# Performance work log

Hardware: AMD Instinct MI355X
Metric: run time of the kernel (lower is better)

## Reference

```python
import jax, jax.numpy as jnp
import numpy as np

B, D = 500000, 128
UNITS, STACK, NPRED = 4, 12, 2
EPS = 1e-3  # Keras BatchNormalization default epsilon


def setup_inputs() -> dict:
    key = jax.random.key(0)
    ks = jax.random.split(key, 2 * STACK + 4)
    inp = {"x": jax.random.normal(ks[0], (B, D), dtype=jnp.float32)}
    # 12 dense weights with growing input width D + 4*i
    for i in range(STACK):
        inp[f"w{i}"] = jax.random.normal(ks[1 + i], (D + UNITS * i, UNITS), dtype=jnp.float32) * 0.1
    inp["gamma"] = 1.0 + 0.1 * jax.random.normal(ks[STACK + 1], (STACK, UNITS), dtype=jnp.float32)
    inp["beta"] = 0.1 * jax.random.normal(ks[STACK + 2], (STACK, UNITS), dtype=jnp.float32)
    inp["mean"] = 0.1 * jax.random.normal(ks[STACK + 3], (STACK, UNITS), dtype=jnp.float32)
    inp["var"] = 0.5 + jax.random.uniform(ks[2 * STACK], (STACK, UNITS), dtype=jnp.float32)
    inp["wf"] = jax.random.normal(ks[2 * STACK + 1], (D + UNITS * STACK, NPRED), dtype=jnp.float32) * 0.1
    inp["bf"] = jnp.zeros((NPRED,), dtype=jnp.float32)
    return inp


def reference(x, w0, w1, w2, w3, w4, w5, w6, w7, w8, w9, w10, w11,
              gamma, beta, mean, var, wf, bf):
    ws = [w0, w1, w2, w3, w4, w5, w6, w7, w8, w9, w10, w11]
    h = x
    for i in range(STACK):
        y = h @ ws[i]  # [B, 4]
        # inference-mode BatchNorm, fused scale/shift
        scale = gamma[i] * jax.lax.rsqrt(var[i] + EPS)
        y = jax.nn.relu(y * scale + (beta[i] - mean[i] * scale))
        h = jnp.concatenate([y, h], axis=-1)  # width grows by 4
    logits = h @ wf + bf  # [B, 2]
    return jax.nn.softmax(logits, axis=-1)
```

## Files before the change

### kernel.cpp

```cpp
#include <hip/hip_runtime.h>

#define NROWS 500000
#define DD 128
#define NSTACK 12
#define BNEPS 1e-3f
#define NCOL 50
#define NTILES ((NROWS + 63) / 64)

typedef float  v2f    __attribute__((ext_vector_type(2)));
typedef float  v4f    __attribute__((ext_vector_type(4)));
typedef float  f32x4  __attribute__((ext_vector_type(4)));
typedef __bf16 bf16x8 __attribute__((ext_vector_type(8)));

__device__ __forceinline__ unsigned short f2bf_rn(float f) {
    unsigned u = __float_as_uint(f);
    return (unsigned short)((u + 0x7FFFu + ((u >> 16) & 1u)) >> 16);
}

__global__ __launch_bounds__(256, 3) void gemm_kernel(
    const float* __restrict__ x,
    const float* __restrict__ w0,  const float* __restrict__ w1,
    const float* __restrict__ w2,  const float* __restrict__ w3,
    const float* __restrict__ w4,  const float* __restrict__ w5,
    const float* __restrict__ w6,  const float* __restrict__ w7,
    const float* __restrict__ w8,  const float* __restrict__ w9,
    const float* __restrict__ w10, const float* __restrict__ w11,
    const float* __restrict__ wf,
    float* __restrict__ T)
{
    __shared__ __align__(16) unsigned short bsw[4][4][64][8];

    const int tid = threadIdx.x;
    const float* ws[NSTACK] = {w0,w1,w2,w3,w4,w5,w6,w7,w8,w9,w10,w11};

    for (int idx = tid; idx < 1024; idx += 256)
        ((f32x4*)&bsw[0][0][0][0])[idx] = (f32x4){0.f, 0.f, 0.f, 0.f};
    __syncthreads();

#pragma unroll
    for (int i = 0; i < NSTACK; ++i) {
        const float* wsi = ws[i];
        for (int e = tid; e < 512; e += 256) {
            const int k = e >> 2, u = e & 3;
            const int n = 4 * i + u;
            const int kt = k >> 5, q = (k >> 3) & 3, j = k & 7;
            const int nt = n >> 4, lane = q * 16 + (n & 15);
            bsw[kt][nt][lane][j] = f2bf_rn(wsi[16 * i + e]);
        }
    }
    {
        const int e = tid;
        const int k = e >> 1, u = e & 1;
        const int n = 48 + u;
        const int kt = k >> 5, q = (k >> 3) & 3, j = k & 7;
        const int lane = q * 16 + (n & 15);
        bsw[kt][3][lane][j] = f2bf_rn(wf[96 + e]);
    }
    __syncthreads();

    const int lane = tid & 63;
    const int wv   = tid >> 6;
    const int tile = blockIdx.x * 4 + wv;
    const int rowbase = tile * 64;
    const int m = lane & 15;
    const int q = lane >> 4;

    const float* arow[4];
#pragma unroll
    for (int mt = 0; mt < 4; ++mt) {
        int r = rowbase + mt * 16 + m;
        if (r > NROWS - 1) r = NROWS - 1;
        arow[mt] = x + (size_t)r * DD + q * 8;
    }

    f32x4 acc[4][4];
#pragma unroll
    for (int mt = 0; mt < 4; ++mt)
#pragma unroll
        for (int nt = 0; nt < 4; ++nt) acc[mt][nt] = (f32x4){0.f, 0.f, 0.f, 0.f};

    v4f A0[2][4], A1[2][4];
#pragma unroll
    for (int mt = 0; mt < 4; ++mt) {
        A0[0][mt] = *(const v4f*)(arow[mt]);
        A1[0][mt] = *(const v4f*)(arow[mt] + 4);
    }

#pragma unroll
    for (int kt = 0; kt < 4; ++kt) {
        const int cur = kt & 1, nxt = cur ^ 1;
        if (kt < 3) {
#pragma unroll
            for (int mt = 0; mt < 4; ++mt) {
                A0[nxt][mt] = *(const v4f*)(arow[mt] + (kt + 1) * 32);
                A1[nxt][mt] = *(const v4f*)(arow[mt] + (kt + 1) * 32 + 4);
            }
        }
        bf16x8 bfrag[4];
#pragma unroll
        for (int nt = 0; nt < 4; ++nt)
            bfrag[nt] = *(const bf16x8*)&bsw[kt][nt][lane][0];
#pragma unroll
        for (int mt = 0; mt < 4; ++mt) {
            union { unsigned short us[8]; bf16x8 bv; } au;
#pragma unroll
            for (int e = 0; e < 4; ++e) {
                au.us[e]     = f2bf_rn(A0[cur][mt][e]);
                au.us[4 + e] = f2bf_rn(A1[cur][mt][e]);
            }
#pragma unroll
            for (int nt = 0; nt < 4; ++nt)
                acc[mt][nt] = __builtin_amdgcn_mfma_f32_16x16x32_bf16(
                    au.bv, bfrag[nt], acc[mt][nt], 0, 0, 0);
        }
    }

    float* tb = T + (size_t)tile * 4096;
#pragma unroll
    for (int nt = 0; nt < 4; ++nt) {
        const int c = nt * 16 + m;
        if (c < NCOL) {
#pragma unroll
            for (int mt = 0; mt < 4; ++mt)
                *(v4f*)(tb + c * 64 + mt * 16 + q * 4) = acc[mt][nt];
        }
    }
}

__global__ __launch_bounds__(256, 4) void recur_kernel(
    const float* __restrict__ T,
    const float* __restrict__ w0,  const float* __restrict__ w1,
    const float* __restrict__ w2,  const float* __restrict__ w3,
    const float* __restrict__ w4,  const float* __restrict__ w5,
    const float* __restrict__ w6,  const float* __restrict__ w7,
    const float* __restrict__ w8,  const float* __restrict__ w9,
    const float* __restrict__ w10, const float* __restrict__ w11,
    const float* __restrict__ gamma_, const float* __restrict__ beta_,
    const float* __restrict__ mean_,  const float* __restrict__ var_,
    const float* __restrict__ wf,     const float* __restrict__ bf,
    float* __restrict__ out)
{
    const int row = blockIdx.x * blockDim.x + threadIdx.x;
    if (row >= NROWS) return;

    const float* ws[NSTACK] = {w0,w1,w2,w3,w4,w5,w6,w7,w8,w9,w10,w11};

    const int tile = row >> 6, rr = row & 63;
    const float* tb = T + (size_t)tile * 4096 + rr;

    float Tv[NCOL];
#pragma unroll
    for (int c = 0; c < NCOL; ++c) Tv[c] = tb[c * 64];

    float y[NSTACK * 4];
#pragma unroll
    for (int i = 0; i < NSTACK; ++i) {
        float a0 = Tv[4 * i + 0], a1 = Tv[4 * i + 1];
        float a2 = Tv[4 * i + 2], a3 = Tv[4 * i + 3];
        const float* wsi = ws[i];
#pragma unroll
        for (int mr = 0; mr < 4 * i; ++mr) {
            const float hv = y[(i - 1 - (mr >> 2)) * 4 + (mr & 3)];
            a0 += hv * wsi[4 * mr + 0];
            a1 += hv * wsi[4 * mr + 1];
            a2 += hv * wsi[4 * mr + 2];
            a3 += hv * wsi[4 * mr + 3];
        }
#pragma unroll
        for (int u = 0; u < 4; ++u) {
            const float sc = gamma_[4 * i + u] * __frsqrt_rn(var_[4 * i + u] + BNEPS);
            const float sh = beta_[4 * i + u] - mean_[4 * i + u] * sc;
            const float a  = (u == 0 ? a0 : u == 1 ? a1 : u == 2 ? a2 : a3);
            const float v  = a * sc + sh;
            y[4 * i + u] = v > 0.f ? v : 0.f;
        }
    }

    float l0 = Tv[48] + bf[0];
    float l1 = Tv[49] + bf[1];
#pragma unroll
    for (int mr = 0; mr < 48; ++mr) {
        const float hv = y[(11 - (mr >> 2)) * 4 + (mr & 3)];
        l0 += hv * wf[2 * mr + 0];
        l1 += hv * wf[2 * mr + 1];
    }

    const float mx = fmaxf(l0, l1);
    const float e0 = __expf(l0 - mx);
    const float e1 = __expf(l1 - mx);
    const float inv = 1.0f / (e0 + e1);
    *(v2f*)(out + (size_t)row * 2) = (v2f){e0 * inv, e1 * inv};
}

extern "C" void kernel_launch(void* const* d_in, const int* in_sizes, int n_in,
                              void* d_out, int out_size, void* d_ws, size_t ws_size,
                              hipStream_t stream) {
    const float* x   = (const float*)d_in[0];
    const float* w0  = (const float*)d_in[1];
    const float* w1  = (const float*)d_in[2];
    const float* w2  = (const float*)d_in[3];
    const float* w3  = (const float*)d_in[4];
    const float* w4  = (const float*)d_in[5];
    const float* w5  = (const float*)d_in[6];
    const float* w6  = (const float*)d_in[7];
    const float* w7  = (const float*)d_in[8];
    const float* w8  = (const float*)d_in[9];
    const float* w9  = (const float*)d_in[10];
    const float* w10 = (const float*)d_in[11];
    const float* w11 = (const float*)d_in[12];
    const float* gm  = (const float*)d_in[13];
    const float* bt  = (const float*)d_in[14];
    const float* mn  = (const float*)d_in[15];
    const float* vr  = (const float*)d_in[16];
    const float* wf  = (const float*)d_in[17];
    const float* bf  = (const float*)d_in[18];
    float* out = (float*)d_out;
    float* T   = (float*)d_ws;

    {
        dim3 block(256);
        dim3 grid((NTILES + 3) / 4);
        hipLaunchKernelGGL(gemm_kernel, grid, block, 0, stream,
                           x, w0, w1, w2, w3, w4, w5, w6, w7, w8, w9, w10, w11,
                           wf, T);
    }
    {
        dim3 block(256);
        dim3 grid((NROWS + 255) / 256);
        hipLaunchKernelGGL(recur_kernel, grid, block, 0, stream,
                           T, w0, w1, w2, w3, w4, w5, w6, w7, w8, w9, w10, w11,
                           gm, bt, mn, vr, wf, bf, out);
    }
}
```

Baseline: 447.6 us.

## Fuse GEMM and recurrence into one persistent kernel with LDS transpose

Merges the MFMA projection kernel and the per-row recurrence kernel into a single persistent kernel, so the 50-column intermediate for each 64-row tile goes through shared memory instead of a global workspace round trip. A tiny prep kernel converts the weights into the bf16 fragment layout once and precomputes the BatchNorm scale/shift, so each block only copies them. The fused kernel grid-strides over tiles with a fixed block count. In exchange it drops the software prefetch of x, and the serial recurrence now runs in the same waves as the GEMM, which may reduce latency hiding and occupancy.

```diff
diff --git a/kernel.cpp b/kernel.cpp
--- a/kernel.cpp
+++ b/kernel.cpp
@@ -6,6 +6,8 @@
 #define BNEPS 1e-3f
 #define NCOL 50
 #define NTILES ((NROWS + 63) / 64)
+#define NBLOCKS 768
+#define TRS 50
 
 typedef float  v2f    __attribute__((ext_vector_type(2)));
 typedef float  v4f    __attribute__((ext_vector_type(4)));
@@ -17,118 +19,7 @@
     return (unsigned short)((u + 0x7FFFu + ((u >> 16) & 1u)) >> 16);
 }
 
-__global__ __launch_bounds__(256, 3) void gemm_kernel(
-    const float* __restrict__ x,
-    const float* __restrict__ w0,  const float* __restrict__ w1,
-    const float* __restrict__ w2,  const float* __restrict__ w3,
-    const float* __restrict__ w4,  const float* __restrict__ w5,
-    const float* __restrict__ w6,  const float* __restrict__ w7,
-    const float* __restrict__ w8,  const float* __restrict__ w9,
-    const float* __restrict__ w10, const float* __restrict__ w11,
-    const float* __restrict__ wf,
-    float* __restrict__ T)
-{
-    __shared__ __align__(16) unsigned short bsw[4][4][64][8];
-
-    const int tid = threadIdx.x;
-    const float* ws[NSTACK] = {w0,w1,w2,w3,w4,w5,w6,w7,w8,w9,w10,w11};
-
-    for (int idx = tid; idx < 1024; idx += 256)
-        ((f32x4*)&bsw[0][0][0][0])[idx] = (f32x4){0.f, 0.f, 0.f, 0.f};
-    __syncthreads();
-
-#pragma unroll
-    for (int i = 0; i < NSTACK; ++i) {
-        const float* wsi = ws[i];
-        for (int e = tid; e < 512; e += 256) {
-            const int k = e >> 2, u = e & 3;
-            const int n = 4 * i + u;
-            const int kt = k >> 5, q = (k >> 3) & 3, j = k & 7;
-            const int nt = n >> 4, lane = q * 16 + (n & 15);
-            bsw[kt][nt][lane][j] = f2bf_rn(wsi[16 * i + e]);
-        }
-    }
-    {
-        const int e = tid;
-        const int k = e >> 1, u = e & 1;
-        const int n = 48 + u;
-        const int kt = k >> 5, q = (k >> 3) & 3, j = k & 7;
-        const int lane = q * 16 + (n & 15);
-        bsw[kt][3][lane][j] = f2bf_rn(wf[96 + e]);
-    }
-    __syncthreads();
-
-    const int lane = tid & 63;
-    const int wv   = tid >> 6;
-    const int tile = blockIdx.x * 4 + wv;
-    const int rowbase = tile * 64;
-    const int m = lane & 15;
-    const int q = lane >> 4;
-
-    const float* arow[4];
-#pragma unroll
-    for (int mt = 0; mt < 4; ++mt) {
-        int r = rowbase + mt * 16 + m;
-        if (r > NROWS - 1) r = NROWS - 1;
-        arow[mt] = x + (size_t)r * DD + q * 8;
-    }
-
-    f32x4 acc[4][4];
-#pragma unroll
-    for (int mt = 0; mt < 4; ++mt)
-#pragma unroll
-        for (int nt = 0; nt < 4; ++nt) acc[mt][nt] = (f32x4){0.f, 0.f, 0.f, 0.f};
-
-    v4f A0[2][4], A1[2][4];
-#pragma unroll
-    for (int mt = 0; mt < 4; ++mt) {
-        A0[0][mt] = *(const v4f*)(arow[mt]);
-        A1[0][mt] = *(const v4f*)(arow[mt] + 4);
-    }
-
-#pragma unroll
-    for (int kt = 0; kt < 4; ++kt) {
-        const int cur = kt & 1, nxt = cur ^ 1;
-        if (kt < 3) {
-#pragma unroll
-            for (int mt = 0; mt < 4; ++mt) {
-                A0[nxt][mt] = *(const v4f*)(arow[mt] + (kt + 1) * 32);
-                A1[nxt][mt] = *(const v4f*)(arow[mt] + (kt + 1) * 32 + 4);
-            }
-        }
-        bf16x8 bfrag[4];
-#pragma unroll
-        for (int nt = 0; nt < 4; ++nt)
-            bfrag[nt] = *(const bf16x8*)&bsw[kt][nt][lane][0];
-#pragma unroll
-        for (int mt = 0; mt < 4; ++mt) {
-            union { unsigned short us[8]; bf16x8 bv; } au;
-#pragma unroll
-            for (int e = 0; e < 4; ++e) {
-                au.us[e]     = f2bf_rn(A0[cur][mt][e]);
-                au.us[4 + e] = f2bf_rn(A1[cur][mt][e]);
-            }
-#pragma unroll
-            for (int nt = 0; nt < 4; ++nt)
-                acc[mt][nt] = __builtin_amdgcn_mfma_f32_16x16x32_bf16(
-                    au.bv, bfrag[nt], acc[mt][nt], 0, 0, 0);
-        }
-    }
-
-    float* tb = T + (size_t)tile * 4096;
-#pragma unroll
-    for (int nt = 0; nt < 4; ++nt) {
-        const int c = nt * 16 + m;
-        if (c < NCOL) {
-#pragma unroll
-            for (int mt = 0; mt < 4; ++mt)
-                *(v4f*)(tb + c * 64 + mt * 16 + q * 4) = acc[mt][nt];
-        }
-    }
-}
-
-__global__ __launch_bounds__(256, 4) void recur_kernel(
-    const float* __restrict__ T,
+__global__ __launch_bounds__(256) void prep_kernel(
     const float* __restrict__ w0,  const float* __restrict__ w1,
     const float* __restrict__ w2,  const float* __restrict__ w3,
     const float* __restrict__ w4,  const float* __restrict__ w5,
@@ -137,59 +28,193 @@
     const float* __restrict__ w10, const float* __restrict__ w11,
     const float* __restrict__ gamma_, const float* __restrict__ beta_,
     const float* __restrict__ mean_,  const float* __restrict__ var_,
-    const float* __restrict__ wf,     const float* __restrict__ bf,
+    const float* __restrict__ wf,
+    unsigned short* __restrict__ gbsw, float* __restrict__ scsh)
+{
+    const int tid = threadIdx.x;
+    const float* ws[NSTACK] = {w0,w1,w2,w3,w4,w5,w6,w7,w8,w9,w10,w11};
+
+    for (int idx = tid; idx < 1024; idx += 256)
+        ((f32x4*)gbsw)[idx] = (f32x4){0.f, 0.f, 0.f, 0.f};
+    __syncthreads();
+
+#pragma unroll
+    for (int i = 0; i < NSTACK; ++i) {
+        const float* wsi = ws[i];
+        for (int e = tid; e < 512; e += 256) {
+            const int k = e >> 2, u = e & 3;
+            const int n = 4 * i + u;
+            const int kt = k >> 5, q = (k >> 3) & 3, j = k & 7;
+            const int nt = n >> 4, lane = q * 16 + (n & 15);
+            gbsw[((kt * 4 + nt) * 64 + lane) * 8 + j] = f2bf_rn(wsi[16 * i + e]);
+        }
+    }
+    {
+        const int e = tid;
+        const int k = e >> 1, u = e & 1;
+        const int n = 48 + u;
+        const int kt = k >> 5, q = (k >> 3) & 3, j = k & 7;
+        const int lane = q * 16 + (n & 15);
+        gbsw[((kt * 4 + 3) * 64 + lane) * 8 + j] = f2bf_rn(wf[96 + e]);
+    }
+    if (tid < 48) {
+        const float sc = gamma_[tid] * __frsqrt_rn(var_[tid] + BNEPS);
+        scsh[tid]      = sc;
+        scsh[48 + tid] = beta_[tid] - mean_[tid] * sc;
+    }
+}
+
+__global__ __launch_bounds__(256, 3) void predict_kernel(
+    const float* __restrict__ x,
+    const unsigned short* __restrict__ gbsw,
+    const float* __restrict__ scsh,
+    const float* __restrict__ w0,  const float* __restrict__ w1,
+    const float* __restrict__ w2,  const float* __restrict__ w3,
+    const float* __restrict__ w4,  const float* __restrict__ w5,
+    const float* __restrict__ w6,  const float* __restrict__ w7,
+    const float* __restrict__ w8,  const float* __restrict__ w9,
+    const float* __restrict__ w10, const float* __restrict__ w11,
+    const float* __restrict__ wf,  const float* __restrict__ bf,
     float* __restrict__ out)
 {
-    const int row = blockIdx.x * blockDim.x + threadIdx.x;
-    if (row >= NROWS) return;
+    __shared__ __align__(16) unsigned short bsw[4][4][64][8];
+    __shared__ __align__(16) float trow[4][32 * TRS];
+
+    const int tid = threadIdx.x;
+    for (int idx = tid; idx < 1024; idx += 256)
+        ((f32x4*)&bsw[0][0][0][0])[idx] = ((const f32x4*)gbsw)[idx];
+    __syncthreads();
 
     const float* ws[NSTACK] = {w0,w1,w2,w3,w4,w5,w6,w7,w8,w9,w10,w11};
-
-    const int tile = row >> 6, rr = row & 63;
-    const float* tb = T + (size_t)tile * 4096 + rr;
-
-    float Tv[NCOL];
-#pragma unroll
-    for (int c = 0; c < NCOL; ++c) Tv[c] = tb[c * 64];
-
-    float y[NSTACK * 4];
-#pragma unroll
-    for (int i = 0; i < NSTACK; ++i) {
-        float a0 = Tv[4 * i + 0], a1 = Tv[4 * i + 1];
-        float a2 = Tv[4 * i + 2], a3 = Tv[4 * i + 3];
-        const float* wsi = ws[i];
-#pragma unroll
-        for (int mr = 0; mr < 4 * i; ++mr) {
-            const float hv = y[(i - 1 - (mr >> 2)) * 4 + (mr & 3)];
-            a0 += hv * wsi[4 * mr + 0];
-            a1 += hv * wsi[4 * mr + 1];
-            a2 += hv * wsi[4 * mr + 2];
-            a3 += hv * wsi[4 * mr + 3];
-        }
-#pragma unroll
-        for (int u = 0; u < 4; ++u) {
-            const float sc = gamma_[4 * i + u] * __frsqrt_rn(var_[4 * i + u] + BNEPS);
-            const float sh = beta_[4 * i + u] - mean_[4 * i + u] * sc;
-            const float a  = (u == 0 ? a0 : u == 1 ? a1 : u == 2 ? a2 : a3);
-            const float v  = a * sc + sh;
-            y[4 * i + u] = v > 0.f ? v : 0.f;
-        }
-    }
-
-    float l0 = Tv[48] + bf[0];
-    float l1 = Tv[49] + bf[1];
-#pragma unroll
-    for (int mr = 0; mr < 48; ++mr) {
-        const float hv = y[(11 - (mr >> 2)) * 4 + (mr & 3)];
-        l0 += hv * wf[2 * mr + 0];
-        l1 += hv * wf[2 * mr + 1];
-    }
-
-    const float mx = fmaxf(l0, l1);
-    const float e0 = __expf(l0 - mx);
-    const float e1 = __expf(l1 - mx);
-    const float inv = 1.0f / (e0 + e1);
-    *(v2f*)(out + (size_t)row * 2) = (v2f){e0 * inv, e1 * inv};
+    const int lane = tid & 63;
+    const int wv   = tid >> 6;
+    const int m = lane & 15;
+    const int q = lane >> 4;
+    const int slots = NBLOCKS * 4;
+    float* wtr = &trow[wv][0];
+
+    for (int tile = blockIdx.x * 4 + wv; tile < NTILES; tile += slots) {
+        const int rowbase = tile * 64;
+
+        const float* arow[4];
+#pragma unroll
+        for (int mt = 0; mt < 4; ++mt) {
+            int r = rowbase + mt * 16 + m;
+            if (r > NROWS - 1) r = NROWS - 1;
+            arow[mt] = x + (size_t)r * DD + q * 8;
+        }
+
+        f32x4 acc[4][4];
+#pragma unroll
+        for (int mt = 0; mt < 4; ++mt)
+#pragma unroll
+            for (int nt = 0; nt < 4; ++nt) acc[mt][nt] = (f32x4){0.f, 0.f, 0.f, 0.f};
+
+#pragma unroll
+        for (int kt = 0; kt < 4; ++kt) {
+            bf16x8 bfrag[4];
+#pragma unroll
+            for (int nt = 0; nt < 4; ++nt)
+                bfrag[nt] = *(const bf16x8*)&bsw[kt][nt][lane][0];
+#pragma unroll
+            for (int mt = 0; mt < 4; ++mt) {
+                const v4f a0 = *(const v4f*)(arow[mt] + kt * 32);
+                const v4f a1 = *(const v4f*)(arow[mt] + kt * 32 + 4);
+                union { unsigned short us[8]; bf16x8 bv; } au;
+#pragma unroll
+                for (int e = 0; e < 4; ++e) {
+                    au.us[e]     = f2bf_rn(a0[e]);
+                    au.us[4 + e] = f2bf_rn(a1[e]);
+                }
+#pragma unroll
+                for (int nt = 0; nt < 4; ++nt)
+                    acc[mt][nt] = __builtin_amdgcn_mfma_f32_16x16x32_bf16(
+                        au.bv, bfrag[nt], acc[mt][nt], 0, 0, 0);
+            }
+        }
+
+        float T[NCOL];
+#pragma unroll
+        for (int mt = 0; mt < 2; ++mt)
+#pragma unroll
+            for (int nt = 0; nt < 4; ++nt) {
+                const int c = nt * 16 + m;
+                if (c < NCOL) {
+#pragma unroll
+                    for (int r = 0; r < 4; ++r)
+                        wtr[(mt * 16 + q * 4 + r) * TRS + c] = acc[mt][nt][r];
+                }
+            }
+        if (lane < 32) {
+            const float* tb = wtr + lane * TRS;
+#pragma unroll
+            for (int j = 0; j < NCOL / 2; ++j) {
+                const v2f t = *(const v2f*)(tb + 2 * j);
+                T[2 * j] = t.x; T[2 * j + 1] = t.y;
+            }
+        }
+#pragma unroll
+        for (int mt = 2; mt < 4; ++mt)
+#pragma unroll
+            for (int nt = 0; nt < 4; ++nt) {
+                const int c = nt * 16 + m;
+                if (c < NCOL) {
+#pragma unroll
+                    for (int r = 0; r < 4; ++r)
+                        wtr[((mt - 2) * 16 + q * 4 + r) * TRS + c] = acc[mt][nt][r];
+                }
+            }
+        if (lane >= 32) {
+            const float* tb = wtr + (lane - 32) * TRS;
+#pragma unroll
+            for (int j = 0; j < NCOL / 2; ++j) {
+                const v2f t = *(const v2f*)(tb + 2 * j);
+                T[2 * j] = t.x; T[2 * j + 1] = t.y;
+            }
+        }
+
+        float y[NSTACK * 4];
+#pragma unroll
+        for (int i = 0; i < NSTACK; ++i) {
+            float a0 = T[4 * i + 0], a1 = T[4 * i + 1];
+            float a2 = T[4 * i + 2], a3 = T[4 * i + 3];
+            const float* wsi = ws[i];
+#pragma unroll
+            for (int mr = 0; mr < 4 * i; ++mr) {
+                const float hv = y[(i - 1 - (mr >> 2)) * 4 + (mr & 3)];
+                a0 += hv * wsi[4 * mr + 0];
+                a1 += hv * wsi[4 * mr + 1];
+                a2 += hv * wsi[4 * mr + 2];
+                a3 += hv * wsi[4 * mr + 3];
+            }
+#pragma unroll
+            for (int u = 0; u < 4; ++u) {
+                const float sc = scsh[4 * i + u];
+                const float sh = scsh[48 + 4 * i + u];
+                const float a  = (u == 0 ? a0 : u == 1 ? a1 : u == 2 ? a2 : a3);
+                const float v  = a * sc + sh;
+                y[4 * i + u] = v > 0.f ? v : 0.f;
+            }
+        }
+
+        float l0 = T[48] + bf[0];
+        float l1 = T[49] + bf[1];
+#pragma unroll
+        for (int mr = 0; mr < 48; ++mr) {
+            const float hv = y[(11 - (mr >> 2)) * 4 + (mr & 3)];
+            l0 += hv * wf[2 * mr + 0];
+            l1 += hv * wf[2 * mr + 1];
+        }
+
+        const float mx = fmaxf(l0, l1);
+        const float e0 = __expf(l0 - mx);
+        const float e1 = __expf(l1 - mx);
+        const float inv = 1.0f / (e0 + e1);
+
+        const int row = rowbase + lane;
+        if (row < NROWS)
+            *(v2f*)(out + (size_t)row * 2) = (v2f){e0 * inv, e1 * inv};
+    }
 }
 
 extern "C" void kernel_launch(void* const* d_in, const int* in_sizes, int n_in,
@@ -215,20 +240,16 @@
     const float* wf  = (const float*)d_in[17];
     const float* bf  = (const float*)d_in[18];
     float* out = (float*)d_out;
-    float* T   = (float*)d_ws;
-
-    {
-        dim3 block(256);
-        dim3 grid((NTILES + 3) / 4);
-        hipLaunchKernelGGL(gemm_kernel, grid, block, 0, stream,
-                           x, w0, w1, w2, w3, w4, w5, w6, w7, w8, w9, w10, w11,
-                           wf, T);
-    }
-    {
-        dim3 block(256);
-        dim3 grid((NROWS + 255) / 256);
-        hipLaunchKernelGGL(recur_kernel, grid, block, 0, stream,
-                           T, w0, w1, w2, w3, w4, w5, w6, w7, w8, w9, w10, w11,
-                           gm, bt, mn, vr, wf, bf, out);
-    }
-}
+
+    unsigned short* gbsw = (unsigned short*)d_ws;
+    float*          scsh = (float*)((char*)d_ws + 16384);
+
+    hipLaunchKernelGGL(prep_kernel, dim3(1), dim3(256), 0, stream,
+                       w0, w1, w2, w3, w4, w5, w6, w7, w8, w9, w10, w11,
+                       gm, bt, mn, vr, wf, gbsw, scsh);
+
+    hipLaunchKernelGGL(predict_kernel, dim3(NBLOCKS), dim3(256), 0, stream,
+                       x, gbsw, scsh,
+                       w0, w1, w2, w3, w4, w5, w6, w7, w8, w9, w10, w11,
+                       wf, bf, out);
+}
```

Result: faster. 420.2 us (-6.1%).
